# Kernel tuning notes

Measured on AMD Instinct MI355X. Metric: run time of the kernel, lower is better.

Reference implementation:

```python
import jax, jax.numpy as jnp
import numpy as np

L, N, D_IN = 4, 2048, 1024
H, DH = 8, 64
INNER = H * DH          # 512
D_OUT = D_IN            # out_dim defaults to input_dim
SCALE = DH ** -0.5


def setup_inputs() -> dict:
    key = jax.random.key(0)
    ks = jax.random.split(key, 7)
    x = jax.random.normal(ks[0], (L, N, D_IN), jnp.float32)
    # torch Linear weights are [out_features, in_features]; xavier-ish scale
    Wq = jax.random.normal(ks[1], (INNER, D_IN), jnp.float32) * 0.03
    Wk = jax.random.normal(ks[2], (INNER, D_IN), jnp.float32) * 0.03
    Wv = jax.random.normal(ks[3], (INNER, D_IN), jnp.float32) * 0.03
    Wo = jax.random.normal(ks[4], (D_OUT, INNER), jnp.float32) * 0.03
    bo = jnp.zeros((D_OUT,), jnp.float32)
    # boolean key-padding mask [L, n]; ensure at least one valid key per row
    mask = jax.random.uniform(ks[5], (L, N)) < 0.9
    mask = mask.at[:, 0].set(True)
    return {"x": x, "Wq": Wq, "Wk": Wk, "Wv": Wv, "Wo": Wo, "bo": bo, "mask": mask}


def reference(x, Wq, Wk, Wv, Wo, bo, mask):
    # projections (Linear: y = x @ W^T), split heads: L n (h d) -> l h n d
    def split_heads(t):
        return t.reshape(L, N, H, DH).transpose(0, 2, 1, 3)

    q = split_heads(jnp.einsum('lnd,ed->lne', x, Wq))
    k = split_heads(jnp.einsum('lnd,ed->lne', x, Wk))  # context defaults to x
    v = split_heads(jnp.einsum('lnd,ed->lne', x, Wv))

    sim = jnp.einsum('lhnd,lhmd->lhnm', q, k) * SCALE   # [L,H,N,N]
    neg = -jnp.finfo(sim.dtype).max
    sim = jnp.where(mask[:, None, None, :], sim, neg)   # mask over key dim
    attn = jax.nn.softmax(sim, axis=-1)

    out = jnp.einsum('lhnm,lhmd->lhnd', attn, v)        # [L,H,N,DH]
    out = out.transpose(0, 2, 1, 3).reshape(L, N, INNER)
    return out @ Wo.T + bo                               # [L,N,D_OUT]
```

## Files before the change

kernel.cpp:

```cpp
#include <hip/hip_runtime.h>
#include <hip/hip_bf16.h>

#define L_DIM 4
#define N_DIM 2048
#define DIN   1024
#define H_DIM 8
#define DH    64
#define INNER 512

typedef __attribute__((ext_vector_type(8))) short short8;
typedef __attribute__((ext_vector_type(4))) float f32x4;

__device__ __forceinline__ unsigned short f2bf(float f) {
  unsigned u = __builtin_bit_cast(unsigned, f);
  u += 0x7fffu + ((u >> 16) & 1u);
  return (unsigned short)(u >> 16);
}

__device__ __forceinline__ unsigned pack2(float a, float b) {
  unsigned ua = __builtin_bit_cast(unsigned, a) + 0x8000u;
  unsigned ub = __builtin_bit_cast(unsigned, b) + 0x8000u;
  return (ua >> 16) | (ub & 0xffff0000u);
}

typedef __attribute__((address_space(3))) unsigned int lds_uint;
typedef const __attribute__((address_space(1))) unsigned int glob_uint;
__device__ __forceinline__ void gl_lds16(const unsigned short* g,
                                         unsigned short* l) {
  __builtin_amdgcn_global_load_lds((glob_uint*)g, (lds_uint*)l, 16, 0, 0);
}

__global__ void cast_all(const float* __restrict__ x,
                         const float* __restrict__ wq,
                         const float* __restrict__ wk,
                         const float* __restrict__ wv,
                         const float* __restrict__ wo,
                         unsigned short* __restrict__ xb,
                         unsigned short* __restrict__ w3,
                         unsigned short* __restrict__ wob,
                         const unsigned char* __restrict__ mraw,
                         float* __restrict__ bias) {
  __shared__ int votes[2];
  int bid = blockIdx.x, t = threadIdx.x;
  if (bid == 10240) {
    if (t < 2) votes[t] = 0;
    __syncthreads();
    const unsigned int* m32 = (const unsigned int*)mraw;
    int anyf = 0, any8 = 0;
    for (int i = t; i < 2048; i += 256) {
      unsigned w = m32[i];
      if (w == 0x3f800000u) anyf = 1;
      if (w & 0xffffff00u) any8 = 1;
    }
    if (anyf) atomicOr(&votes[0], 1);
    if (any8) atomicOr(&votes[1], 1);
    __syncthreads();
    int fmt = votes[0] ? 2 : (votes[1] ? 1 : 0);
    for (int i = t; i < L_DIM * N_DIM; i += 256) {
      int mv;
      if (fmt == 2)      mv = ((const float*)mraw)[i] != 0.0f;
      else if (fmt == 1) mv = mraw[i] != 0;
      else               mv = ((const int*)mraw)[i] != 0;
      bias[i] = mv ? 0.0f : -1e30f;
    }
    return;
  }
  int i = (bid * 256 + t) * 4;
  const float* src; unsigned short* dst; int off;
  if (i < 8388608)      { src = x;  dst = xb;           off = i; }
  else if (i < 8912896) { src = wq; dst = w3;           off = i - 8388608; }
  else if (i < 9437184) { src = wk; dst = w3 + 524288;  off = i - 8912896; }
  else if (i < 9961472) { src = wv; dst = w3 + 1048576; off = i - 9437184; }
  else                  { src = wo; dst = wob;          off = i - 9961472; }
  float4 f = *(const float4*)(src + off);
  ushort4 o4;
  o4.x = f2bf(f.x); o4.y = f2bf(f.y); o4.z = f2bf(f.z); o4.w = f2bf(f.w);
  *(ushort4*)(dst + off) = o4;
}

__launch_bounds__(256, 3)
__global__ void gemm_qkv(const unsigned short* __restrict__ xb,
                         const unsigned short* __restrict__ w3,
                         unsigned short* __restrict__ qp,
                         unsigned short* __restrict__ kp,
                         unsigned short* __restrict__ vtp) {
  __shared__ __align__(16) unsigned short Sh[8704];
  unsigned short* As = Sh;
  unsigned short* Bs = Sh + 4096;
  const int tid = threadIdx.x, lane = tid & 63, wid = tid >> 6;
  const int l16 = lane & 15, quad = lane >> 4;
  const int wm = wid >> 1, wn = wid & 1;
  const int m0 = blockIdx.x * 128, n0 = blockIdx.y * 128;

  f32x4 acc[4][4] = {};
  for (int kt = 0; kt < DIN; kt += 32) {
    __syncthreads();
#pragma unroll
    for (int it = 0; it < 2; ++it) {
      int c = it * 256 + wid * 64 + lane;
      int row = c >> 2, kseg = c & 3;
      unsigned short* lbase = &As[(it * 256 + wid * 64) * 8];
      gl_lds16(&xb[(m0 + row) * DIN + kt + kseg * 8], lbase);
      unsigned short* lbase2 = &Bs[(it * 256 + wid * 64) * 8];
      gl_lds16(&w3[(n0 + row) * DIN + kt + kseg * 8], lbase2);
    }
    __syncthreads();
    short8 af[4], bf[4];
#pragma unroll
    for (int mt = 0; mt < 4; ++mt)
      af[mt] = *(const short8*)&As[(wm * 64 + mt * 16 + l16) * 32 + quad * 8];
#pragma unroll
    for (int nt = 0; nt < 4; ++nt)
      bf[nt] = *(const short8*)&Bs[(wn * 64 + nt * 16 + l16) * 32 + quad * 8];
#pragma unroll
    for (int mt = 0; mt < 4; ++mt)
#pragma unroll
      for (int nt = 0; nt < 4; ++nt)
        acc[mt][nt] = __builtin_amdgcn_mfma_f32_16x16x32_bf16(
            af[mt], bf[nt], acc[mt][nt], 0, 0, 0);
  }
  if (blockIdx.y >= 8) {
    const int l = m0 >> 11, mloc = m0 & 2047;
#pragma unroll
    for (int chunk = 0; chunk < 2; ++chunk) {
      __syncthreads();
      if (wn == chunk) {
#pragma unroll
        for (int mt = 0; mt < 4; ++mt)
#pragma unroll
          for (int nt = 0; nt < 4; ++nt) {
            int col = nt * 16 + l16;
            int rowb = wm * 64 + mt * 16 + quad * 4;
            ushort4 pv;
            pv.x = f2bf(acc[mt][nt][0]);
            pv.y = f2bf(acc[mt][nt][1]);
            pv.z = f2bf(acc[mt][nt][2]);
            pv.w = f2bf(acc[mt][nt][3]);
            *(ushort4*)&Sh[col * 136 + rowb] = pv;
          }
      }
      __syncthreads();
      int hh = ((n0 + chunk * 64) & 511) >> 6;
#pragma unroll
      for (int it = 0; it < 4; ++it) {
        int c = it * 256 + tid;
        int cl = c >> 4, seg = c & 15;
        short8 vv = *(const short8*)&Sh[cl * 136 + seg * 8];
        *(short8*)&vtp[((size_t)((l * H_DIM + hh) * DH + cl)) * N_DIM + mloc +
                       seg * 8] = vv;
      }
    }
  } else {
#pragma unroll
    for (int mt = 0; mt < 4; ++mt)
#pragma unroll
      for (int nt = 0; nt < 4; ++nt)
#pragma unroll
        for (int r = 0; r < 4; ++r) {
          int grow = m0 + wm * 64 + mt * 16 + quad * 4 + r;
          int gcol = n0 + wn * 64 + nt * 16 + l16;
          unsigned short bv = f2bf(acc[mt][nt][r]);
          int h = (gcol & 511) >> 6, d = gcol & 63;
          int l = grow >> 11, n = grow & 2047;
          unsigned short* dst = (gcol >> 9) ? kp : qp;
          dst[(((l * H_DIM + h) * N_DIM + n) * DH) + d] = bv;
        }
  }
}

#define PW_S 64
__launch_bounds__(256, 2)
__global__ void attn_kernel(const unsigned short* __restrict__ qg,
                            const unsigned short* __restrict__ kg,
                            const unsigned short* __restrict__ vtg,
                            const float* __restrict__ bias,
                            unsigned short* __restrict__ aout) {
  __shared__ __align__(16) unsigned short Ks[2][128 * 64];
  __shared__ __align__(16) unsigned short Vs[2][64 * 128];
  __shared__ __align__(16) unsigned short Pw[128 * PW_S];
  const int tid = threadIdx.x, lane = tid & 63, wid = tid >> 6;
  const int l16 = lane & 15, quad = lane >> 4;
  const int bid = blockIdx.x;
  const int xcd = bid & 7, j = bid >> 3;
  const int lh = xcd * 4 + (j >> 4);
  const int q0 = (j & 15) << 7;
  const int l = lh >> 3, h = lh & 7;
  const unsigned short* Qb = qg + (size_t)lh * N_DIM * DH;
  const unsigned short* Kb = kg + (size_t)lh * N_DIM * DH;
  const unsigned short* Vt = vtg + (size_t)lh * DH * N_DIM;
  const float* bl = bias + l * N_DIM;

  short8 qf[2][2];
#pragma unroll
  for (int mt = 0; mt < 2; ++mt)
#pragma unroll
    for (int ks = 0; ks < 2; ++ks)
      qf[mt][ks] = *(const short8*)&Qb[(q0 + wid * 32 + mt * 16 + l16) * DH +
                                       ks * 32 + quad * 8];

  f32x4 o[2][4] = {};
  float lsum[2] = {0.f, 0.f};

#pragma unroll
  for (int it = 0; it < 4; ++it) {
    int cb = it * 256 + wid * 64;
    int c = cb + lane;
    int key = c >> 3, sl = c & 7, gs = (sl + key) & 7;
    gl_lds16(&Kb[key * DH + gs * 8], &Ks[0][cb * 8]);
    int d = c >> 4, sv = c & 15, gv = (sv + d) & 15;
    gl_lds16(&Vt[(size_t)d * N_DIM + gv * 8], &Vs[0][cb * 8]);
  }

  for (int t = 0; t < 16; ++t) {
    const int kv = t << 7, buf = t & 1;
    __syncthreads();
    if (t < 15) {
      int kv2 = kv + 128, b2 = buf ^ 1;
#pragma unroll
      for (int it = 0; it < 4; ++it) {
        int cb = it * 256 + wid * 64;
        int c = cb + lane;
        int key = c >> 3, sl = c & 7, gs = (sl + key) & 7;
        gl_lds16(&Kb[(kv2 + key) * DH + gs * 8], &Ks[b2][cb * 8]);
        int d = c >> 4, sv = c & 15, gv = (sv + d) & 15;
        gl_lds16(&Vt[(size_t)d * N_DIM + kv2 + gv * 8], &Vs[b2][cb * 8]);
      }
    }
    const unsigned short* Kst = Ks[buf];
    const unsigned short* Vst = Vs[buf];

#pragma unroll
    for (int hf = 0; hf < 2; ++hf) {
      f32x4 sc[2][4] = {};
#pragma unroll
      for (int nt = 0; nt < 4; ++nt)
#pragma unroll
        for (int ks = 0; ks < 2; ++ks) {
          int s = (ks * 4 + quad - l16) & 7;
          short8 kf = *(const short8*)&Kst[(hf * 64 + nt * 16 + l16) * 64 +
                                           s * 8];
#pragma unroll
          for (int mt = 0; mt < 2; ++mt)
            sc[mt][nt] = __builtin_amdgcn_mfma_f32_16x16x32_bf16(
                kf, qf[mt][ks], sc[mt][nt], 0, 0, 0);
        }
#pragma unroll
      for (int mt = 0; mt < 2; ++mt) {
        unsigned short* pr = &Pw[(wid * 32 + mt * 16 + l16) * PW_S];
#pragma unroll
        for (int nt = 0; nt < 4; ++nt) {
          float4 b4 = *(const float4*)&bl[kv + hf * 64 + nt * 16 + quad * 4];
          float p0 = __expf(fmaf(sc[mt][nt][0], 0.125f, b4.x));
          float p1 = __expf(fmaf(sc[mt][nt][1], 0.125f, b4.y));
          float p2 = __expf(fmaf(sc[mt][nt][2], 0.125f, b4.z));
          float p3 = __expf(fmaf(sc[mt][nt][3], 0.125f, b4.w));
          lsum[mt] += (p0 + p1) + (p2 + p3);
          uint2 pk = make_uint2(pack2(p0, p1), pack2(p2, p3));
          int gk = nt * 2 + (quad >> 1);
          int s = (gk + l16) & 7;
          *(uint2*)&pr[s * 8 + (quad & 1) * 4] = pk;
        }
      }
#pragma unroll
      for (int g = 0; g < 2; ++g) {
        short8 pa[2];
#pragma unroll
        for (int mt = 0; mt < 2; ++mt) {
          int sp = (g * 4 + quad + l16) & 7;
          pa[mt] = *(const short8*)&Pw[(wid * 32 + mt * 16 + l16) * PW_S +
                                       sp * 8];
        }
#pragma unroll
        for (int nt = 0; nt < 4; ++nt) {
          int dd = nt * 16 + l16;
          int sv2 = (hf * 8 + g * 4 + quad - l16) & 15;
          short8 vb = *(const short8*)&Vst[dd * 128 + sv2 * 8];
#pragma unroll
          for (int mt = 0; mt < 2; ++mt)
            o[mt][nt] = __builtin_amdgcn_mfma_f32_16x16x32_bf16(
                pa[mt], vb, o[mt][nt], 0, 0, 0);
        }
      }
    }
  }
#pragma unroll
  for (int mt = 0; mt < 2; ++mt) {
    lsum[mt] += __shfl_xor(lsum[mt], 16);
    lsum[mt] += __shfl_xor(lsum[mt], 32);
  }
#pragma unroll
  for (int mt = 0; mt < 2; ++mt)
#pragma unroll
    for (int r = 0; r < 4; ++r) {
      float inv = 1.f / __shfl(lsum[mt], quad * 4 + r);
      int row = q0 + wid * 32 + mt * 16 + quad * 4 + r;
#pragma unroll
      for (int nt = 0; nt < 4; ++nt)
        aout[(size_t)(l * N_DIM + row) * INNER + h * DH + nt * 16 + l16] =
            f2bf(o[mt][nt][r] * inv);
    }
}

__launch_bounds__(256, 3)
__global__ void gemm_out(const unsigned short* __restrict__ a,
                         const unsigned short* __restrict__ wo,
                         const float* __restrict__ bo,
                         float* __restrict__ out) {
  __shared__ unsigned short As[128 * 32];
  __shared__ unsigned short Bs[128 * 32];
  const int tid = threadIdx.x, lane = tid & 63, wid = tid >> 6;
  const int l16 = lane & 15, quad = lane >> 4;
  const int wm = wid >> 1, wn = wid & 1;
  const int m0 = blockIdx.x * 128, n0 = blockIdx.y * 128;

  f32x4 acc[4][4] = {};
  for (int kt = 0; kt < INNER; kt += 32) {
    __syncthreads();
#pragma unroll
    for (int it = 0; it < 2; ++it) {
      int c = it * 256 + wid * 64 + lane;
      int row = c >> 2, kseg = c & 3;
      unsigned short* lbase = &As[(it * 256 + wid * 64) * 8];
      gl_lds16(&a[(m0 + row) * INNER + kt + kseg * 8], lbase);
      unsigned short* lbase2 = &Bs[(it * 256 + wid * 64) * 8];
      gl_lds16(&wo[(n0 + row) * INNER + kt + kseg * 8], lbase2);
    }
    __syncthreads();
    short8 af[4], bf[4];
#pragma unroll
    for (int mt = 0; mt < 4; ++mt)
      af[mt] = *(const short8*)&As[(wm * 64 + mt * 16 + l16) * 32 + quad * 8];
#pragma unroll
    for (int nt = 0; nt < 4; ++nt)
      bf[nt] = *(const short8*)&Bs[(wn * 64 + nt * 16 + l16) * 32 + quad * 8];
#pragma unroll
    for (int mt = 0; mt < 4; ++mt)
#pragma unroll
      for (int nt = 0; nt < 4; ++nt)
        acc[mt][nt] = __builtin_amdgcn_mfma_f32_16x16x32_bf16(
            af[mt], bf[nt], acc[mt][nt], 0, 0, 0);
  }
#pragma unroll
  for (int mt = 0; mt < 4; ++mt)
#pragma unroll
    for (int nt = 0; nt < 4; ++nt)
#pragma unroll
      for (int r = 0; r < 4; ++r) {
        int grow = m0 + wm * 64 + mt * 16 + quad * 4 + r;
        int gcol = n0 + wn * 64 + nt * 16 + l16;
        out[(size_t)grow * DIN + gcol] = acc[mt][nt][r] + bo[gcol];
      }
}

extern "C" void kernel_launch(void* const* d_in, const int* in_sizes, int n_in,
                              void* d_out, int out_size, void* d_ws,
                              size_t ws_size, hipStream_t stream) {
  const float* x  = (const float*)d_in[0];
  const float* Wq = (const float*)d_in[1];
  const float* Wk = (const float*)d_in[2];
  const float* Wv = (const float*)d_in[3];
  const float* Wo = (const float*)d_in[4];
  const float* bo = (const float*)d_in[5];
  const unsigned char* mask = (const unsigned char*)d_in[6];
  float* out = (float*)d_out;

  char* ws = (char*)d_ws;
  unsigned short* xb  = (unsigned short*)(ws + 0);
  unsigned short* w3  = (unsigned short*)(ws + 16777216);
  unsigned short* wob = (unsigned short*)(ws + 19922944);
  unsigned short* q   = (unsigned short*)(ws + 20971520);
  unsigned short* k   = (unsigned short*)(ws + 29360128);
  unsigned short* vt  = (unsigned short*)(ws + 37748736);
  unsigned short* att = (unsigned short*)(ws + 46137344);
  float* bias         = (float*)(ws + 54525952);

  cast_all<<<10241, 256, 0, stream>>>(x, Wq, Wk, Wv, Wo, xb, w3, wob, mask,
                                      bias);
  gemm_qkv<<<dim3(64, 12), 256, 0, stream>>>(xb, w3, q, k, vt);
  attn_kernel<<<512, 256, 0, stream>>>(q, k, vt, bias, att);
  gemm_out<<<dim3(64, 8), 256, 0, stream>>>(att, wob, bo, out);
}
```

Baseline: 213.9 us.

## Shrink attention tiles to 64 rows/keys and use native exp2 and packed bf16 conversion

The attention kernel now runs 1024 blocks of two waves, each handling 64 query rows and iterating over 64-key K/V tiles, instead of 512 four-wave blocks with 128-row, 128-key tiles. LDS use per block drops, so more blocks can be resident and the grid fills the machine more evenly. The cost is more loop trips and barriers per block and less K/V reuse across query rows. The softmax exponent now uses v_exp_f32 with log2e folded into the scale, the bf16 packing uses v_cvt_pk_bf16_f32, and the K/V load offsets are precomputed outside the loop.

```diff
diff --git a/kernel.cpp b/kernel.cpp
--- a/kernel.cpp
+++ b/kernel.cpp
@@ -17,10 +17,16 @@
   return (unsigned short)(u >> 16);
 }
 
-__device__ __forceinline__ unsigned pack2(float a, float b) {
-  unsigned ua = __builtin_bit_cast(unsigned, a) + 0x8000u;
-  unsigned ub = __builtin_bit_cast(unsigned, b) + 0x8000u;
-  return (ua >> 16) | (ub & 0xffff0000u);
+__device__ __forceinline__ unsigned cvtpk(float a, float b) {
+  unsigned r;
+  asm("v_cvt_pk_bf16_f32 %0, %1, %2" : "=v"(r) : "v"(a), "v"(b));
+  return r;
+}
+
+__device__ __forceinline__ float fexp2(float x) {
+  float r;
+  asm("v_exp_f32 %0, %1" : "=v"(r) : "v"(x));
+  return r;
 }
 
 typedef __attribute__((address_space(3))) unsigned int lds_uint;
@@ -169,21 +175,21 @@
 }
 
 #define PW_S 64
-__launch_bounds__(256, 2)
+__launch_bounds__(128, 2)
 __global__ void attn_kernel(const unsigned short* __restrict__ qg,
                             const unsigned short* __restrict__ kg,
                             const unsigned short* __restrict__ vtg,
                             const float* __restrict__ bias,
                             unsigned short* __restrict__ aout) {
-  __shared__ __align__(16) unsigned short Ks[2][128 * 64];
-  __shared__ __align__(16) unsigned short Vs[2][64 * 128];
-  __shared__ __align__(16) unsigned short Pw[128 * PW_S];
+  __shared__ __align__(16) unsigned short Ks[2][64 * 64];
+  __shared__ __align__(16) unsigned short Vs[2][64 * 64];
+  __shared__ __align__(16) unsigned short Pw[64 * PW_S];
   const int tid = threadIdx.x, lane = tid & 63, wid = tid >> 6;
   const int l16 = lane & 15, quad = lane >> 4;
   const int bid = blockIdx.x;
   const int xcd = bid & 7, j = bid >> 3;
-  const int lh = xcd * 4 + (j >> 4);
-  const int q0 = (j & 15) << 7;
+  const int lh = xcd * 4 + (j >> 5);
+  const int q0 = (j & 31) << 6;
   const int l = lh >> 3, h = lh & 7;
   const unsigned short* Qb = qg + (size_t)lh * N_DIM * DH;
   const unsigned short* Kb = kg + (size_t)lh * N_DIM * DH;
@@ -201,85 +207,84 @@
   f32x4 o[2][4] = {};
   float lsum[2] = {0.f, 0.f};
 
+  int kof[4], ldsb[4];
+  size_t vof[4];
 #pragma unroll
   for (int it = 0; it < 4; ++it) {
-    int cb = it * 256 + wid * 64;
-    int c = cb + lane;
-    int key = c >> 3, sl = c & 7, gs = (sl + key) & 7;
-    gl_lds16(&Kb[key * DH + gs * 8], &Ks[0][cb * 8]);
-    int d = c >> 4, sv = c & 15, gv = (sv + d) & 15;
-    gl_lds16(&Vt[(size_t)d * N_DIM + gv * 8], &Vs[0][cb * 8]);
-  }
-
-  for (int t = 0; t < 16; ++t) {
-    const int kv = t << 7, buf = t & 1;
-    __syncthreads();
-    if (t < 15) {
-      int kv2 = kv + 128, b2 = buf ^ 1;
+    int cb = it * 128 + wid * 64, c = cb + lane;
+    int rr = c >> 3, sl = c & 7, gs = (sl + rr) & 7;
+    kof[it] = rr * DH + gs * 8;
+    vof[it] = (size_t)rr * N_DIM + gs * 8;
+    ldsb[it] = cb * 8;
+  }
+
+#pragma unroll
+  for (int it = 0; it < 4; ++it) {
+    gl_lds16(&Kb[kof[it]], &Ks[0][ldsb[it]]);
+    gl_lds16(&Vt[vof[it]], &Vs[0][ldsb[it]]);
+  }
+
+  for (int t = 0; t < 32; ++t) {
+    const int kv = t << 6, buf = t & 1;
+    __syncthreads();
+    if (t < 31) {
+      int kv2 = kv + 64, b2 = buf ^ 1;
 #pragma unroll
       for (int it = 0; it < 4; ++it) {
-        int cb = it * 256 + wid * 64;
-        int c = cb + lane;
-        int key = c >> 3, sl = c & 7, gs = (sl + key) & 7;
-        gl_lds16(&Kb[(kv2 + key) * DH + gs * 8], &Ks[b2][cb * 8]);
-        int d = c >> 4, sv = c & 15, gv = (sv + d) & 15;
-        gl_lds16(&Vt[(size_t)d * N_DIM + kv2 + gv * 8], &Vs[b2][cb * 8]);
+        gl_lds16(&Kb[(kv2 << 6) + kof[it]], &Ks[b2][ldsb[it]]);
+        gl_lds16(&Vt[vof[it] + kv2], &Vs[b2][ldsb[it]]);
       }
     }
     const unsigned short* Kst = Ks[buf];
     const unsigned short* Vst = Vs[buf];
 
-#pragma unroll
-    for (int hf = 0; hf < 2; ++hf) {
-      f32x4 sc[2][4] = {};
-#pragma unroll
-      for (int nt = 0; nt < 4; ++nt)
-#pragma unroll
-        for (int ks = 0; ks < 2; ++ks) {
-          int s = (ks * 4 + quad - l16) & 7;
-          short8 kf = *(const short8*)&Kst[(hf * 64 + nt * 16 + l16) * 64 +
-                                           s * 8];
-#pragma unroll
-          for (int mt = 0; mt < 2; ++mt)
-            sc[mt][nt] = __builtin_amdgcn_mfma_f32_16x16x32_bf16(
-                kf, qf[mt][ks], sc[mt][nt], 0, 0, 0);
-        }
+    f32x4 sc[2][4] = {};
+#pragma unroll
+    for (int nt = 0; nt < 4; ++nt)
+#pragma unroll
+      for (int ks = 0; ks < 2; ++ks) {
+        int s = (ks * 4 + quad - l16) & 7;
+        short8 kf = *(const short8*)&Kst[(nt * 16 + l16) * 64 + s * 8];
+#pragma unroll
+        for (int mt = 0; mt < 2; ++mt)
+          sc[mt][nt] = __builtin_amdgcn_mfma_f32_16x16x32_bf16(
+              kf, qf[mt][ks], sc[mt][nt], 0, 0, 0);
+      }
+#pragma unroll
+    for (int mt = 0; mt < 2; ++mt) {
+      unsigned short* pr = &Pw[(wid * 32 + mt * 16 + l16) * PW_S];
+#pragma unroll
+      for (int nt = 0; nt < 4; ++nt) {
+        float4 b4 = *(const float4*)&bl[kv + nt * 16 + quad * 4];
+        float p0 = fexp2(fmaf(sc[mt][nt][0], 0.18033688011f, b4.x));
+        float p1 = fexp2(fmaf(sc[mt][nt][1], 0.18033688011f, b4.y));
+        float p2 = fexp2(fmaf(sc[mt][nt][2], 0.18033688011f, b4.z));
+        float p3 = fexp2(fmaf(sc[mt][nt][3], 0.18033688011f, b4.w));
+        lsum[mt] += (p0 + p1) + (p2 + p3);
+        uint2 pk = make_uint2(cvtpk(p0, p1), cvtpk(p2, p3));
+        int gk = nt * 2 + (quad >> 1);
+        int s = (gk + l16) & 7;
+        *(uint2*)&pr[s * 8 + (quad & 1) * 4] = pk;
+      }
+    }
+#pragma unroll
+    for (int g = 0; g < 2; ++g) {
+      short8 pa[2];
 #pragma unroll
       for (int mt = 0; mt < 2; ++mt) {
-        unsigned short* pr = &Pw[(wid * 32 + mt * 16 + l16) * PW_S];
-#pragma unroll
-        for (int nt = 0; nt < 4; ++nt) {
-          float4 b4 = *(const float4*)&bl[kv + hf * 64 + nt * 16 + quad * 4];
-          float p0 = __expf(fmaf(sc[mt][nt][0], 0.125f, b4.x));
-          float p1 = __expf(fmaf(sc[mt][nt][1], 0.125f, b4.y));
-          float p2 = __expf(fmaf(sc[mt][nt][2], 0.125f, b4.z));
-          float p3 = __expf(fmaf(sc[mt][nt][3], 0.125f, b4.w));
-          lsum[mt] += (p0 + p1) + (p2 + p3);
-          uint2 pk = make_uint2(pack2(p0, p1), pack2(p2, p3));
-          int gk = nt * 2 + (quad >> 1);
-          int s = (gk + l16) & 7;
-          *(uint2*)&pr[s * 8 + (quad & 1) * 4] = pk;
-        }
-      }
-#pragma unroll
-      for (int g = 0; g < 2; ++g) {
-        short8 pa[2];
-#pragma unroll
-        for (int mt = 0; mt < 2; ++mt) {
-          int sp = (g * 4 + quad + l16) & 7;
-          pa[mt] = *(const short8*)&Pw[(wid * 32 + mt * 16 + l16) * PW_S +
-                                       sp * 8];
-        }
-#pragma unroll
-        for (int nt = 0; nt < 4; ++nt) {
-          int dd = nt * 16 + l16;
-          int sv2 = (hf * 8 + g * 4 + quad - l16) & 15;
-          short8 vb = *(const short8*)&Vst[dd * 128 + sv2 * 8];
-#pragma unroll
-          for (int mt = 0; mt < 2; ++mt)
-            o[mt][nt] = __builtin_amdgcn_mfma_f32_16x16x32_bf16(
-                pa[mt], vb, o[mt][nt], 0, 0, 0);
-        }
+        int sp = (g * 4 + quad + l16) & 7;
+        pa[mt] = *(const short8*)&Pw[(wid * 32 + mt * 16 + l16) * PW_S +
+                                     sp * 8];
+      }
+#pragma unroll
+      for (int nt = 0; nt < 4; ++nt) {
+        int dd = nt * 16 + l16;
+        int sv2 = (g * 4 + quad - l16) & 7;
+        short8 vb = *(const short8*)&Vst[dd * 64 + sv2 * 8];
+#pragma unroll
+        for (int mt = 0; mt < 2; ++mt)
+          o[mt][nt] = __builtin_amdgcn_mfma_f32_16x16x32_bf16(
+              pa[mt], vb, o[mt][nt], 0, 0, 0);
       }
     }
   }
@@ -377,6 +382,6 @@
   cast_all<<<10241, 256, 0, stream>>>(x, Wq, Wk, Wv, Wo, xb, w3, wob, mask,
                                       bias);
   gemm_qkv<<<dim3(64, 12), 256, 0, stream>>>(xb, w3, q, k, vt);
-  attn_kernel<<<512, 256, 0, stream>>>(q, k, vt, bias, att);
+  attn_kernel<<<1024, 128, 0, stream>>>(q, k, vt, bias, att);
   gemm_out<<<dim3(64, 8), 256, 0, stream>>>(att, wob, bo, out);
 }
```

Result: no change. 214.8 us (+0.4%).
